# Performance work log

Hardware: AMD Instinct MI355X
Metric: run time of the kernel (lower is better)

The kernel has to match this reference:

```python
import jax, jax.numpy as jnp
import numpy as np

N, IN_DIM, HID, HEADS, OUT64, OUT_DIM, E = 10000, 512, 64, 8, 64, 5000, 160000
NEG_SLOPE = 0.2


def gatv2_layer(x, src, dst, Wl, bl, Wr, br, att, bias, heads, ch, concat):
    n = x.shape[0]
    xl = (x @ Wl.T + bl).reshape(n, heads, ch)  # source transform
    xr = (x @ Wr.T + br).reshape(n, heads, ch)  # target transform
    h = xl[src] + xr[dst]                       # [E, H, C]
    e = jnp.einsum('ehc,hc->eh', jax.nn.leaky_relu(h, NEG_SLOPE), att)
    # segment softmax over destination nodes (every node has a self-loop)
    m = jax.ops.segment_max(e, dst, num_segments=n)
    a = jnp.exp(e - m[dst])
    s = jax.ops.segment_sum(a, dst, num_segments=n)
    alpha = a / (s[dst] + 1e-16)                # [E, H]
    msg = xl[src] * alpha[..., None]            # [E, H, C]
    out = jax.ops.segment_sum(msg, dst, num_segments=n)  # [N, H, C]
    if concat:
        return out.reshape(n, heads * ch) + bias
    return out.mean(axis=1) + bias


def setup_inputs() -> dict:
    key = jax.random.key(0)
    ks = jax.random.split(key, 16)
    def glorot(k, shape):
        fan_in, fan_out = shape[-1], shape[0]
        lim = jnp.sqrt(6.0 / (fan_in + fan_out))
        return jax.random.uniform(k, shape, jnp.float32, -lim, lim)
    x = jax.random.normal(ks[0], (N, IN_DIM), jnp.float32)
    edge_index = jax.random.randint(ks[1], (2, E), 0, N, jnp.int64)
    return {
        'x': x,
        'edge_index': edge_index,
        'W1l': glorot(ks[2], (HEADS * HID, IN_DIM)),
        'b1l': jnp.zeros((HEADS * HID,), jnp.float32),
        'W1r': glorot(ks[3], (HEADS * HID, IN_DIM)),
        'b1r': jnp.zeros((HEADS * HID,), jnp.float32),
        'att1': glorot(ks[4], (HEADS, HID)),
        'bias1': jnp.zeros((HEADS * HID,), jnp.float32),
        'W2l': glorot(ks[5], (OUT64, HEADS * HID)),
        'b2l': jnp.zeros((OUT64,), jnp.float32),
        'W2r': glorot(ks[6], (OUT64, HEADS * HID)),
        'b2r': jnp.zeros((OUT64,), jnp.float32),
        'att2': glorot(ks[7], (1, OUT64)),
        'bias2': jnp.zeros((OUT64,), jnp.float32),
        'fc_w': glorot(ks[8], (OUT_DIM, OUT64)),
        'fc_b': jnp.zeros((OUT_DIM,), jnp.float32),
    }


def reference(x, edge_index, W1l, b1l, W1r, b1r, att1, bias1,
              W2l, b2l, W2r, b2r, att2, bias2, fc_w, fc_b):
    n = x.shape[0]
    loops = jnp.arange(n, dtype=edge_index.dtype)
    src = jnp.concatenate([edge_index[0], loops])  # PyG adds self-loops
    dst = jnp.concatenate([edge_index[1], loops])
    h = gatv2_layer(x, src, dst, W1l, b1l, W1r, b1r, att1, bias1, HEADS, HID, True)
    h = jax.nn.relu(h)  # dropout is identity in eval mode
    h = gatv2_layer(h, src, dst, W2l, b2l, W2r, b2r, att2, bias2, 1, OUT64, False)
    h = jax.nn.relu(h)
    return h @ fc_w.T + fc_b
```

## Files before the change

### kernel.cpp

```cpp
#include <hip/hip_runtime.h>
#include <hip/hip_bf16.h>

#define NN     10000
#define HEADS  8
#define HID    64
#define ODIM   5000
#define NE     160000
#define ET     170000
#define NEG    0.2f
#define WT_LD  5120

__global__ void k_detect(const int* __restrict__ ei, int* __restrict__ flag) {
    __shared__ int nz;
    if (threadIdx.x == 0) nz = 0;
    __syncthreads();
    if (ei[2 * threadIdx.x + 1] != 0) atomicAdd(&nz, 1);
    __syncthreads();
    if (threadIdx.x == 0) *flag = (nz == 0) ? 1 : 0;
}
__device__ __forceinline__ int ld_idx(const int* ei, int k, int mode) {
    return mode ? ei[2 * k] : ei[k];
}

__global__ void k_deg_init(int* __restrict__ deg) {
    int i = blockIdx.x * blockDim.x + threadIdx.x;
    if (i < NN) deg[i] = 1;
}
__global__ void k_hist(const int* __restrict__ ei, const int* __restrict__ flag,
                       int* __restrict__ deg) {
    int e = blockIdx.x * blockDim.x + threadIdx.x;
    if (e < NE) atomicAdd(&deg[ld_idx(ei, NE + e, *flag)], 1);
}
__global__ void k_scan(const int* __restrict__ deg, int* __restrict__ rowptr,
                       int* __restrict__ cursor) {
    __shared__ int sd[1024];
    __shared__ int carry;
    int t = threadIdx.x;
    if (t == 0) carry = 0;
    __syncthreads();
    for (int base = 0; base < NN; base += 1024) {
        int i = base + t;
        int v = (i < NN) ? deg[i] : 0;
        sd[t] = v;
        __syncthreads();
        for (int off = 1; off < 1024; off <<= 1) {
            int x = (t >= off) ? sd[t - off] : 0;
            __syncthreads();
            sd[t] += x;
            __syncthreads();
        }
        if (i < NN) { int ex = carry + sd[t] - v; rowptr[i] = ex; cursor[i] = ex; }
        __syncthreads();
        if (t == 0) carry += sd[1023];
        __syncthreads();
    }
    if (t == 0) rowptr[NN] = carry;
}
__global__ void k_scatter(const int* __restrict__ ei, const int* __restrict__ flag,
                          int* __restrict__ cursor, int* __restrict__ csr) {
    int e = blockIdx.x * blockDim.x + threadIdx.x;
    if (e < NE) {
        int mode = *flag;
        int d = ld_idx(ei, NE + e, mode);
        int pos = atomicAdd(&cursor[d], 1);
        csr[pos] = ld_idx(ei, e, mode);
    } else if (e < ET) {
        int n = e - NE;
        int pos = atomicAdd(&cursor[n], 1);
        csr[pos] = n;
    }
}

__global__ void __launch_bounds__(256) k_gemm_nt(
    const float* __restrict__ A, const float* __restrict__ W,
    const float* __restrict__ bias, float* __restrict__ C,
    int M, int Ndim, int K) {
    __shared__ float As[32][64];
    __shared__ float Ws[32][64];
    int t = threadIdx.x;
    int m0 = blockIdx.x * 64, n0 = blockIdx.y * 64;
    int lm = t >> 2;
    int kc = (t & 3) * 8;
    int tx = t & 15, ty = t >> 4;
    int rowA = m0 + lm;
    int rowW = n0 + lm;
    float acc[4][4] = {};
    for (int kt = 0; kt < K; kt += 32) {
        float av[8];
        if (rowA < M) {
            const float* ap = A + (size_t)rowA * K + kt + kc;
            float4 p0 = *(const float4*)ap;
            float4 p1 = *(const float4*)(ap + 4);
            av[0] = p0.x; av[1] = p0.y; av[2] = p0.z; av[3] = p0.w;
            av[4] = p1.x; av[5] = p1.y; av[6] = p1.z; av[7] = p1.w;
        } else {
            #pragma unroll
            for (int j = 0; j < 8; j++) av[j] = 0.f;
        }
        const float* wp = W + (size_t)rowW * K + kt + kc;
        float4 q0 = *(const float4*)wp;
        float4 q1 = *(const float4*)(wp + 4);
        float wv[8] = {q0.x, q0.y, q0.z, q0.w, q1.x, q1.y, q1.z, q1.w};
        #pragma unroll
        for (int j = 0; j < 8; j++) As[kc + j][lm] = av[j];
        #pragma unroll
        for (int j = 0; j < 8; j++) Ws[kc + j][lm] = wv[j];
        __syncthreads();
        #pragma unroll
        for (int k = 0; k < 32; k++) {
            float4 a4 = *(const float4*)&As[k][ty * 4];
            float4 b4 = *(const float4*)&Ws[k][tx * 4];
            float aa[4] = {a4.x, a4.y, a4.z, a4.w};
            float bb[4] = {b4.x, b4.y, b4.z, b4.w};
            #pragma unroll
            for (int i = 0; i < 4; i++)
                #pragma unroll
                for (int j = 0; j < 4; j++)
                    acc[i][j] = fmaf(aa[i], bb[j], acc[i][j]);
        }
        __syncthreads();
    }
    int col0 = n0 + tx * 4;
    float4 bv = *(const float4*)&bias[col0];
    #pragma unroll
    for (int i = 0; i < 4; i++) {
        int r = m0 + ty * 4 + i;
        if (r < M) {
            float4 o = make_float4(acc[i][0] + bv.x, acc[i][1] + bv.y,
                                   acc[i][2] + bv.z, acc[i][3] + bv.w);
            *(float4*)&C[(size_t)r * Ndim + col0] = o;
        }
    }
}

__global__ void __launch_bounds__(256) k_gat1(
    const float* __restrict__ xl, const float* __restrict__ xr,
    const float* __restrict__ att, const float* __restrict__ bias,
    const int* __restrict__ rowptr, const int* __restrict__ csr,
    float* __restrict__ out) {
    int wid = (blockIdx.x * blockDim.x + threadIdx.x) >> 6;
    int lane = threadIdx.x & 63;
    if (wid >= NN) return;
    int n = wid;
    float xrv[HEADS], atv[HEADS], acc[HEADS], lsum[HEADS], mmax[HEADS];
    #pragma unroll
    for (int h = 0; h < HEADS; h++) {
        int c = h * 64 + lane;
        xrv[h] = xr[(size_t)n * 512 + c];
        atv[h] = att[c];
        acc[h] = 0.f; lsum[h] = 0.f; mmax[h] = -1e30f;
    }
    int p0 = rowptr[n], p1 = rowptr[n + 1];
    for (int p = p0; p < p1; p++) {
        int s = csr[p];
        const float* xlrow = xl + (size_t)s * 512;
        float xs[HEADS], sc[HEADS];
        #pragma unroll
        for (int h = 0; h < HEADS; h++) {
            xs[h] = xlrow[h * 64 + lane];
            float v = xs[h] + xrv[h];
            v = (v > 0.f) ? v : NEG * v;
            sc[h] = v * atv[h];
        }
        #pragma unroll
        for (int h = 0; h < HEADS; h++) {
            float ssum = sc[h];
            #pragma unroll
            for (int off = 32; off > 0; off >>= 1)
                ssum += __shfl_xor(ssum, off, 64);
            sc[h] = ssum;
        }
        #pragma unroll
        for (int h = 0; h < HEADS; h++) {
            float mn = fmaxf(mmax[h], sc[h]);
            float scale = __expf(mmax[h] - mn);
            float pe = __expf(sc[h] - mn);
            acc[h] = acc[h] * scale + pe * xs[h];
            lsum[h] = lsum[h] * scale + pe;
            mmax[h] = mn;
        }
    }
    #pragma unroll
    for (int h = 0; h < HEADS; h++) {
        int c = h * 64 + lane;
        float o = acc[h] / (lsum[h] + 1e-16f) + bias[c];
        out[(size_t)n * 512 + c] = (o > 0.f) ? o : 0.f;
    }
}

__global__ void __launch_bounds__(256) k_gat2(
    const float* __restrict__ xl, const float* __restrict__ xr,
    const float* __restrict__ att, const float* __restrict__ bias,
    const int* __restrict__ rowptr, const int* __restrict__ csr,
    float* __restrict__ out) {
    int wid = (blockIdx.x * blockDim.x + threadIdx.x) >> 6;
    int lane = threadIdx.x & 63;
    if (wid >= NN) return;
    int n = wid;
    float xrv = xr[(size_t)n * 64 + lane];
    float atv = att[lane];
    float acc = 0.f, lsum = 0.f, mmax = -1e30f;
    int p0 = rowptr[n], p1 = rowptr[n + 1];
    for (int p = p0; p < p1; p++) {
        int s = csr[p];
        float xs = xl[(size_t)s * 64 + lane];
        float v = xs + xrv;
        v = (v > 0.f) ? v : NEG * v;
        float sc = v * atv;
        #pragma unroll
        for (int off = 32; off > 0; off >>= 1)
            sc += __shfl_xor(sc, off, 64);
        float mn = fmaxf(mmax, sc);
        float scale = __expf(mmax - mn);
        float pe = __expf(sc - mn);
        acc = acc * scale + pe * xs;
        lsum = lsum * scale + pe;
        mmax = mn;
    }
    float o = acc / (lsum + 1e-16f) + bias[lane];
    out[(size_t)n * 64 + lane] = (o > 0.f) ? o : 0.f;
}

__global__ void __launch_bounds__(256) k_tr(const float* __restrict__ W,
                                            float* __restrict__ Wt) {
    __shared__ float T[64][65];
    int t = threadIdx.x;
    int c0 = blockIdx.x * 64;
    int cl = t >> 2, kq = (t & 3) * 16;
    if (c0 + cl < ODIM) {
        #pragma unroll
        for (int q = 0; q < 4; q++) {
            float4 v = *(const float4*)(W + (size_t)(c0 + cl) * 64 + kq + q * 4);
            T[cl][kq + q * 4 + 0] = v.x;
            T[cl][kq + q * 4 + 1] = v.y;
            T[cl][kq + q * 4 + 2] = v.z;
            T[cl][kq + q * 4 + 3] = v.w;
        }
    } else {
        #pragma unroll
        for (int q = 0; q < 16; q++) T[cl][kq + q] = 0.f;
    }
    __syncthreads();
    int kl = t >> 2, cq = (t & 3) * 16;
    #pragma unroll
    for (int q = 0; q < 4; q++) {
        float4 v = make_float4(T[cq + q * 4 + 0][kl], T[cq + q * 4 + 1][kl],
                               T[cq + q * 4 + 2][kl], T[cq + q * 4 + 3][kl]);
        *(float4*)(Wt + (size_t)kl * WT_LD + c0 + cq + q * 4) = v;
    }
}

__global__ void __launch_bounds__(256) k_fc2(
    const float* __restrict__ A, const float* __restrict__ Wt,
    const float* __restrict__ bias, float* __restrict__ C) {
    __shared__ float As[64][8];
    int t = threadIdx.x;
    int r0 = blockIdx.y * 8;
    int c0 = blockIdx.x * 1024 + t * 4;
    if (t < 128) {
        int r = t >> 4, kq = (t & 15) * 4;
        float4 v = *(const float4*)(A + (size_t)(r0 + r) * 64 + kq);
        As[kq + 0][r] = v.x; As[kq + 1][r] = v.y;
        As[kq + 2][r] = v.z; As[kq + 3][r] = v.w;
    }
    __syncthreads();
    float acc[8][4] = {};
    #pragma unroll 4
    for (int k = 0; k < 64; k++) {
        float4 wv = *(const float4*)(Wt + (size_t)k * WT_LD + c0);
        float4 a0 = *(const float4*)&As[k][0];
        float4 a1 = *(const float4*)&As[k][4];
        float ar[8] = {a0.x, a0.y, a0.z, a0.w, a1.x, a1.y, a1.z, a1.w};
        float wr[4] = {wv.x, wv.y, wv.z, wv.w};
        #pragma unroll
        for (int r = 0; r < 8; r++)
            #pragma unroll
            for (int j = 0; j < 4; j++)
                acc[r][j] = fmaf(ar[r], wr[j], acc[r][j]);
    }
    if (c0 < ODIM) {
        float4 bv = *(const float4*)(bias + c0);
        #pragma unroll
        for (int r = 0; r < 8; r++) {
            float4 o = make_float4(acc[r][0] + bv.x, acc[r][1] + bv.y,
                                   acc[r][2] + bv.z, acc[r][3] + bv.w);
            *(float4*)&C[(size_t)(r0 + r) * ODIM + c0] = o;
        }
    }
}

extern "C" void kernel_launch(void* const* d_in, const int* in_sizes, int n_in,
                              void* d_out, int out_size, void* d_ws, size_t ws_size,
                              hipStream_t stream) {
    const float* x     = (const float*)d_in[0];
    const int*   ei    = (const int*)d_in[1];
    const float* W1l   = (const float*)d_in[2];
    const float* b1l   = (const float*)d_in[3];
    const float* W1r   = (const float*)d_in[4];
    const float* b1r   = (const float*)d_in[5];
    const float* att1  = (const float*)d_in[6];
    const float* bias1 = (const float*)d_in[7];
    const float* W2l   = (const float*)d_in[8];
    const float* b2l   = (const float*)d_in[9];
    const float* W2r   = (const float*)d_in[10];
    const float* b2r   = (const float*)d_in[11];
    const float* att2  = (const float*)d_in[12];
    const float* bias2 = (const float*)d_in[13];
    const float* fcw   = (const float*)d_in[14];
    const float* fcb   = (const float*)d_in[15];
    float* out = (float*)d_out;

    char* p = (char*)d_ws;
    auto carve = [&](size_t bytes) {
        void* r = (void*)p;
        p += (bytes + 255) & ~(size_t)255;
        return r;
    };
    int* deg    = (int*)carve((size_t)NN * 4);
    int* rowptr = (int*)carve((size_t)(NN + 1) * 4);
    int* cursor = (int*)carve((size_t)NN * 4);
    int* csr    = (int*)carve((size_t)ET * 4);
    int* flag   = (int*)carve(256);
    float* Wt  = (float*)carve((size_t)64 * WT_LD * 4);
    float* xl1 = (float*)carve((size_t)NN * 512 * 4);
    float* xr1 = (float*)carve((size_t)NN * 512 * 4);
    float* h1  = (float*)carve((size_t)NN * 512 * 4);
    float* xl2 = xl1;
    float* xr2 = xl1 + (size_t)NN * 64;
    float* h2  = xl1 + (size_t)NN * 128;

    k_detect<<<1, 1024, 0, stream>>>(ei, flag);
    k_tr<<<(ODIM + 63) / 64, 256, 0, stream>>>(fcw, Wt);
    k_deg_init<<<(NN + 255) / 256, 256, 0, stream>>>(deg);
    k_hist<<<(NE + 255) / 256, 256, 0, stream>>>(ei, flag, deg);
    k_scan<<<1, 1024, 0, stream>>>(deg, rowptr, cursor);
    k_scatter<<<(ET + 255) / 256, 256, 0, stream>>>(ei, flag, cursor, csr);

    dim3 g1((NN + 63) / 64, 512 / 64);
    k_gemm_nt<<<g1, 256, 0, stream>>>(x, W1l, b1l, xl1, NN, 512, 512);
    k_gemm_nt<<<g1, 256, 0, stream>>>(x, W1r, b1r, xr1, NN, 512, 512);
    k_gat1<<<(NN * 64 + 255) / 256, 256, 0, stream>>>(xl1, xr1, att1, bias1, rowptr, csr, h1);

    dim3 g2((NN + 63) / 64, 1);
    k_gemm_nt<<<g2, 256, 0, stream>>>(h1, W2l, b2l, xl2, NN, 64, 512);
    k_gemm_nt<<<g2, 256, 0, stream>>>(h1, W2r, b2r, xr2, NN, 64, 512);
    k_gat2<<<(NN * 64 + 255) / 256, 256, 0, stream>>>(xl2, xr2, att2, bias2, rowptr, csr, h2);

    dim3 g3((ODIM + 1023) / 1024, NN / 8);
    k_fc2<<<g3, 256, 0, stream>>>(h2, Wt, fcb, out);
}
```

Baseline: 728.6 us.

## Vectorize GAT layer-1 aggregation with float4 lanes and prefetch next neighbor row

Rewrites the layer-1 attention kernel so each lane owns four contiguous channels in two float4 halves instead of eight strided scalars. A head then spans 16 lanes, so each score reduction needs 4 shuffle steps rather than 6, and there are 2 concurrent score streams per lane instead of 8. The next neighbor's row is loaded before the current one is processed to hide gather latency. The cost is more register pressure and a different lane-to-head mapping, and the kernel now assumes every node has at least one edge (it reads csr[p0] unconditionally).

Result: faster. 649.3 us (-10.9%).

```diff
diff --git a/kernel.cpp b/kernel.cpp
--- a/kernel.cpp
+++ b/kernel.cpp
@@ -142,50 +142,65 @@
     int lane = threadIdx.x & 63;
     if (wid >= NN) return;
     int n = wid;
-    float xrv[HEADS], atv[HEADS], acc[HEADS], lsum[HEADS], mmax[HEADS];
-    #pragma unroll
-    for (int h = 0; h < HEADS; h++) {
-        int c = h * 64 + lane;
-        xrv[h] = xr[(size_t)n * 512 + c];
-        atv[h] = att[c];
-        acc[h] = 0.f; lsum[h] = 0.f; mmax[h] = -1e30f;
-    }
+    int off = lane * 4;
+    const float4* xr4  = (const float4*)(xr + (size_t)n * 512 + off);
+    const float4* att4 = (const float4*)(att + off);
+    float4 xrA = xr4[0],  xrB = xr4[64];
+    float4 atA = att4[0], atB = att4[64];
+    float4 accA = make_float4(0.f, 0.f, 0.f, 0.f);
+    float4 accB = make_float4(0.f, 0.f, 0.f, 0.f);
+    float lA = 0.f, lB = 0.f, mA = -1e30f, mB = -1e30f;
+
     int p0 = rowptr[n], p1 = rowptr[n + 1];
-    for (int p = p0; p < p1; p++) {
-        int s = csr[p];
-        const float* xlrow = xl + (size_t)s * 512;
-        float xs[HEADS], sc[HEADS];
-        #pragma unroll
-        for (int h = 0; h < HEADS; h++) {
-            xs[h] = xlrow[h * 64 + lane];
-            float v = xs[h] + xrv[h];
-            v = (v > 0.f) ? v : NEG * v;
-            sc[h] = v * atv[h];
-        }
-        #pragma unroll
-        for (int h = 0; h < HEADS; h++) {
-            float ssum = sc[h];
-            #pragma unroll
-            for (int off = 32; off > 0; off >>= 1)
-                ssum += __shfl_xor(ssum, off, 64);
-            sc[h] = ssum;
-        }
-        #pragma unroll
-        for (int h = 0; h < HEADS; h++) {
-            float mn = fmaxf(mmax[h], sc[h]);
-            float scale = __expf(mmax[h] - mn);
-            float pe = __expf(sc[h] - mn);
-            acc[h] = acc[h] * scale + pe * xs[h];
-            lsum[h] = lsum[h] * scale + pe;
-            mmax[h] = mn;
-        }
-    }
-    #pragma unroll
-    for (int h = 0; h < HEADS; h++) {
-        int c = h * 64 + lane;
-        float o = acc[h] / (lsum[h] + 1e-16f) + bias[c];
-        out[(size_t)n * 512 + c] = (o > 0.f) ? o : 0.f;
-    }
+    int deg = p1 - p0;
+    const float4* xp = (const float4*)(xl + (size_t)csr[p0] * 512 + off);
+    float4 xa = xp[0], xb = xp[64];
+    for (int i = 0; i < deg; i++) {
+        float4 cxa = xa, cxb = xb;
+        if (i + 1 < deg) {
+            const float4* np = (const float4*)(xl + (size_t)csr[p0 + i + 1] * 512 + off);
+            xa = np[0]; xb = np[64];
+        }
+        float vA0 = cxa.x + xrA.x, vA1 = cxa.y + xrA.y,
+              vA2 = cxa.z + xrA.z, vA3 = cxa.w + xrA.w;
+        float vB0 = cxb.x + xrB.x, vB1 = cxb.y + xrB.y,
+              vB2 = cxb.z + xrB.z, vB3 = cxb.w + xrB.w;
+        vA0 = (vA0 > 0.f) ? vA0 : NEG * vA0;  vA1 = (vA1 > 0.f) ? vA1 : NEG * vA1;
+        vA2 = (vA2 > 0.f) ? vA2 : NEG * vA2;  vA3 = (vA3 > 0.f) ? vA3 : NEG * vA3;
+        vB0 = (vB0 > 0.f) ? vB0 : NEG * vB0;  vB1 = (vB1 > 0.f) ? vB1 : NEG * vB1;
+        vB2 = (vB2 > 0.f) ? vB2 : NEG * vB2;  vB3 = (vB3 > 0.f) ? vB3 : NEG * vB3;
+        float sA = vA0 * atA.x + vA1 * atA.y + vA2 * atA.z + vA3 * atA.w;
+        float sB = vB0 * atB.x + vB1 * atB.y + vB2 * atB.z + vB3 * atB.w;
+        #pragma unroll
+        for (int m = 1; m <= 8; m <<= 1) {
+            sA += __shfl_xor(sA, m, 64);
+            sB += __shfl_xor(sB, m, 64);
+        }
+        float mnA = fmaxf(mA, sA);
+        float scA = __expf(mA - mnA), peA = __expf(sA - mnA);
+        accA.x = accA.x * scA + peA * cxa.x;  accA.y = accA.y * scA + peA * cxa.y;
+        accA.z = accA.z * scA + peA * cxa.z;  accA.w = accA.w * scA + peA * cxa.w;
+        lA = lA * scA + peA;  mA = mnA;
+        float mnB = fmaxf(mB, sB);
+        float scB = __expf(mB - mnB), peB = __expf(sB - mnB);
+        accB.x = accB.x * scB + peB * cxb.x;  accB.y = accB.y * scB + peB * cxb.y;
+        accB.z = accB.z * scB + peB * cxb.z;  accB.w = accB.w * scB + peB * cxb.w;
+        lB = lB * scB + peB;  mB = mnB;
+    }
+    float rA = 1.f / (lA + 1e-16f), rB = 1.f / (lB + 1e-16f);
+    float4 biA = *(const float4*)(bias + off);
+    float4 biB = *(const float4*)(bias + off + 256);
+    float4 oA = make_float4(fmaxf(accA.x * rA + biA.x, 0.f),
+                            fmaxf(accA.y * rA + biA.y, 0.f),
+                            fmaxf(accA.z * rA + biA.z, 0.f),
+                            fmaxf(accA.w * rA + biA.w, 0.f));
+    float4 oB = make_float4(fmaxf(accB.x * rB + biB.x, 0.f),
+                            fmaxf(accB.y * rB + biB.y, 0.f),
+                            fmaxf(accB.z * rB + biB.z, 0.f),
+                            fmaxf(accB.w * rB + biB.w, 0.f));
+    float4* op = (float4*)(out + (size_t)n * 512 + off);
+    op[0]  = oA;
+    op[64] = oB;
 }
 
 __global__ void __launch_bounds__(256) k_gat2(
```
